# Performance work log

Hardware: AMD Instinct MI355X
Metric: run time of the kernel (lower is better)

The kernel has to match this reference:

```python
import jax, jax.numpy as jnp
import numpy as np

EMBED_DIM = 1024
NUM_HEADS = 16
HEAD_DIM = EMBED_DIM // NUM_HEADS

# Hamilton-product combination tensor C[out_comp, weight_comp, in_comp]
_C = np.zeros((4, 4, 4), dtype=np.float32)
for o, terms in enumerate([
    [(0, 0, 1), (1, 1, -1), (2, 2, -1), (3, 3, -1)],  # r_out
    [(1, 0, 1), (0, 1, 1), (3, 2, 1), (2, 3, -1)],    # i_out
    [(2, 0, 1), (3, 1, -1), (0, 2, 1), (1, 3, 1)],    # j_out
    [(3, 0, 1), (2, 1, 1), (1, 2, -1), (0, 3, 1)],    # k_out
]):
    for d, c, s in terms:
        _C[o, d, c] = s
C = jnp.asarray(_C)


def _xavier(key, shape):
    fan_in, fan_out = shape[-1], shape[-2]
    a = jnp.sqrt(6.0 / (fan_in + fan_out))
    return jax.random.uniform(key, shape, jnp.float32, -a, a)


def setup_inputs() -> dict:
    key = jax.random.key(0)
    ks = jax.random.split(key, 8)
    B, T, E = 4, 1024, EMBED_DIM
    inp = {
        'q': jax.random.normal(ks[0], (B, T, E, 4), jnp.float32),
        'k': jax.random.normal(ks[1], (B, T, E, 4), jnp.float32),
        'v': jax.random.normal(ks[2], (B, T, E, 4), jnp.float32),
    }
    for name, kk in zip(['Wq', 'Wk', 'Wv', 'Wo'], ks[3:7]):
        # stacked [r,i,j,k] weights, each (out_features, in_features)
        inp[name] = _xavier(kk, (4, E, E))
        inp[name.replace('W', 'b')] = jnp.zeros((E, 4), jnp.float32)
    return inp


def qlinear(x, W, b):
    # x: [B,T,in,4(c)], W: [4(d),out,in], b: [out,4]
    # effective block weight: Weff[q_out, c_in, out, in]
    Weff = jnp.einsum('doi,qdc->qcoi', W, C)
    out = jnp.einsum('btic,qcoi->btoq', x, Weff)
    return out + b  # bias broadcasts over B,T


def split_heads(x):
    B, T, D, Q = x.shape
    x = x.reshape(B, T, NUM_HEADS, HEAD_DIM, Q)
    return x.transpose(0, 2, 1, 3, 4)  # [B,H,T,hd,4]


def combine_heads(x):
    B, H, T, D, Q = x.shape
    return x.transpose(0, 2, 1, 3, 4).reshape(B, T, H * D, Q)


def reference(q, k, v, Wq, bq, Wk, bk, Wv, bv, Wo, bo):
    qh = split_heads(qlinear(q, Wq, bq))
    kh = split_heads(qlinear(k, Wk, bk))
    vh = split_heads(qlinear(v, Wv, bv))
    scale = 1.0 / jnp.sqrt(jnp.float32(HEAD_DIM * 4))
    scores = jnp.einsum('bhqfd,bhkfd->bhqk', qh, kh) * scale
    attn = jax.nn.softmax(scores, axis=-1)
    out = jnp.einsum('bhqk,bhkfd->bhqfd', attn, vh)
    return qlinear(combine_heads(out), Wo, bo)
```

## Files before the change

### kernel.cpp

```cpp
#include <hip/hip_runtime.h>
#include <hip/hip_bf16.h>

typedef _Float16 h16;
typedef h16   h16x8 __attribute__((ext_vector_type(8)));
typedef h16   h16x4 __attribute__((ext_vector_type(4)));
typedef float f32x4 __attribute__((ext_vector_type(4)));

#define EMB 1024
#define ED4 4096L

__device__ __forceinline__ void gload_lds16(const void* g, void* l) {
    __builtin_amdgcn_global_load_lds(
        (__attribute__((address_space(1))) void*)g,
        (__attribute__((address_space(3))) void*)l,
        16, 0, 0);
}

__global__ __launch_bounds__(256) void k_build_m(const float* __restrict__ W, h16* __restrict__ M) {
    int t = blockIdx.x * 256 + threadIdx.x;
    int i = t & 1023;
    int n = t >> 10;
    int o = n >> 2, q = n & 3;
    unsigned packed = 0xEu | (0x8u << 4) | (0x2u << 8) | (0x4u << 12);
    unsigned sm = (packed >> (q * 4)) & 0xFu;
    h16x4 out;
#pragma unroll
    for (int c = 0; c < 4; ++c) {
        int d = q ^ c;
        float w = W[((long)d * EMB + o) * EMB + i];
        out[c] = (h16)(((sm >> c) & 1u) ? -w : w);
    }
    *(h16x4*)&M[(long)n * ED4 + i * 4] = out;
}

__global__ __launch_bounds__(256) void k_f32_to_f16(const float* __restrict__ in, h16* __restrict__ out) {
    long i = ((long)blockIdx.x * 256 + threadIdx.x) * 4;
    float4 v = *(const float4*)(in + i);
    h16x4 o;
    o[0] = (h16)v.x; o[1] = (h16)v.y; o[2] = (h16)v.z; o[3] = (h16)v.w;
    *(h16x4*)(out + i) = o;
}

#define BAR() __builtin_amdgcn_s_barrier()
#define LGKM0() do { asm volatile("s_waitcnt lgkmcnt(0)" ::: "memory"); \
                     __builtin_amdgcn_sched_barrier(0); } while (0)
#define STAGE(matv, basev, row0v, tt, hh) do { \
    const h16* _src = (basev) + ((row0v) + (hh) * 128L) * 4096L + (long)(tt) * 64 + scol; \
    h16* _dst = &lds[(((tt) & 1) << 15) + (matv) * 16384 + (hh) * 8192 + w * 512]; \
    gload_lds16(_src, _dst); \
    gload_lds16(_src + 64 * 4096L, _dst + 4096); \
} while (0)
#define LDA_(mh, m, ks) (*(const h16x8*)&lds[cb + (mh) * 8192 + (wm * 64 + (m) * 16 + fr) * 64 + ((((ks) * 4 + kq) ^ fr7) << 3)])
#define LDB_(nh, n, ks) (*(const h16x8*)&lds[cb + 16384 + (nh) * 8192 + (wn * 32 + (n) * 16 + fr) * 64 + ((((ks) * 4 + kq) ^ fr7) << 3)])
#define MFMA_Q(MH, NH, BF) do { \
    __builtin_amdgcn_s_setprio(1); \
    _Pragma("unroll") \
    for (int m = 0; m < 4; ++m) \
        _Pragma("unroll") \
        for (int n = 0; n < 2; ++n) { \
            acc[MH][NH][m][n] = __builtin_amdgcn_mfma_f32_16x16x32_f16(af[m][0], BF[n][0], acc[MH][NH][m][n], 0, 0, 0); \
            acc[MH][NH][m][n] = __builtin_amdgcn_mfma_f32_16x16x32_f16(af[m][1], BF[n][1], acc[MH][NH][m][n], 0, 0, 0); \
        } \
    __builtin_amdgcn_s_setprio(0); \
} while (0)

template <typename OUT_T>
__global__ __launch_bounds__(512, 2) void k_gemm256(
    const h16* __restrict__ A, const h16* __restrict__ B,
    OUT_T* __restrict__ C, const float* __restrict__ bias, int nt)
{
    __shared__ __align__(16) h16 lds[65536];

    const int tid = threadIdx.x;
    const int w  = tid >> 6, l = tid & 63;
    const int wm = w >> 2, wn = w & 3;
    const int fr = l & 15, fr7 = l & 7, kq = l >> 4;

    const int srow = w * 8 + (l >> 3);
    const int scol = ((l & 7) ^ ((l >> 3) & 7)) << 3;
    const long arow0 = (long)blockIdx.x * 256 + srow;
    const long brow0 = (long)blockIdx.y * 256 + srow;

    f32x4 acc[2][2][4][2] = {};

    STAGE(0, A, arow0, 0, 0);
    STAGE(1, B, brow0, 0, 0);
    STAGE(0, A, arow0, 0, 1);
    STAGE(1, B, brow0, 0, 1);
    STAGE(0, A, arow0, 1, 0);
    STAGE(1, B, brow0, 1, 0);
    asm volatile("s_waitcnt vmcnt(4)" ::: "memory");
    __builtin_amdgcn_sched_barrier(0);
    BAR();

    for (int t = 0; t < nt; ++t) {
        const int cb = (t & 1) << 15;
        h16x8 af[4][2], b0[2][2], b1[2][2];

#pragma unroll
        for (int m = 0; m < 4; ++m) { af[m][0] = LDA_(0, m, 0); af[m][1] = LDA_(0, m, 1); }
#pragma unroll
        for (int n = 0; n < 2; ++n) { b0[n][0] = LDB_(0, n, 0); b0[n][1] = LDB_(0, n, 1); }
        if (t + 1 < nt) STAGE(0, A, arow0, t + 1, 1);
        BAR(); LGKM0();
        MFMA_Q(0, 0, b0);
        BAR();

#pragma unroll
        for (int n = 0; n < 2; ++n) { b1[n][0] = LDB_(1, n, 0); b1[n][1] = LDB_(1, n, 1); }
        if (t + 1 < nt) STAGE(1, B, brow0, t + 1, 1);
        BAR(); LGKM0();
        MFMA_Q(0, 1, b1);
        BAR();

#pragma unroll
        for (int m = 0; m < 4; ++m) { af[m][0] = LDA_(1, m, 0); af[m][1] = LDA_(1, m, 1); }
        if (t + 2 < nt) STAGE(0, A, arow0, t + 2, 0);
        BAR(); LGKM0();
        MFMA_Q(1, 0, b0);
        BAR();

        if (t + 2 < nt) STAGE(1, B, brow0, t + 2, 0);
        if (t < nt - 2) { asm volatile("s_waitcnt vmcnt(4)" ::: "memory"); }
        else            { asm volatile("s_waitcnt vmcnt(0)" ::: "memory"); }
        __builtin_amdgcn_sched_barrier(0);
        BAR();
        MFMA_Q(1, 1, b1);
        BAR();
    }

    const long row00 = (long)blockIdx.x * 256 + wm * 64 + kq * 4;
    const int  col00 = (int)blockIdx.y * 256 + wn * 32 + fr;
#pragma unroll
    for (int mh = 0; mh < 2; ++mh)
#pragma unroll
        for (int nh = 0; nh < 2; ++nh)
#pragma unroll
            for (int n = 0; n < 2; ++n) {
                const int col = col00 + nh * 128 + n * 16;
                const float bv = bias[col];
#pragma unroll
                for (int m = 0; m < 4; ++m) {
                    const long r0 = row00 + mh * 128 + m * 16;
#pragma unroll
                    for (int j = 0; j < 4; ++j)
                        C[(r0 + j) * 4096L + col] = (OUT_T)(acc[mh][nh][m][n][j] + bv);
                }
            }
}

template <typename OUT_T, bool HAS_BIAS>
__global__ __launch_bounds__(256) void k_gemm_bt(
    const h16* __restrict__ A, const h16* __restrict__ B,
    OUT_T* __restrict__ C, const float* __restrict__ bias,
    int lda, int ldb, int ldc,
    long sAb, long sAh, long sBb, long sBh, long sCb, long sCh,
    float alpha, int kIters)
{
    __shared__ __align__(16) h16 As[128 * 32];
    __shared__ __align__(16) h16 Bs[128 * 32];

    const int z = blockIdx.z, zb = z >> 4, zh = z & 15;
    const h16* Ab = A + zb * sAb + zh * sAh + (long)blockIdx.x * 128 * lda;
    const h16* Bb = B + zb * sBb + zh * sBh + (long)blockIdx.y * 128 * ldb;

    const int tid = threadIdx.x, w = tid >> 6, lane = tid & 63;
    const int wr = (w >> 1) * 64, wc = (w & 1) * 64;
    const int scol = (lane & 3) * 8;
    const int srow = lane >> 2;
    const int koff = (lane >> 4) * 8;
    const int fr   = lane & 15;

    f32x4 acc[4][4] = {};

    for (int kt = 0; kt < kIters; ++kt) {
        const int k0 = kt * 32;
#pragma unroll
        for (int j = 0; j < 2; ++j) {
            const int ca  = w * 2 + j;
            const int row = ca * 16 + srow;
            gload_lds16(Ab + (long)row * lda + k0 + scol, &As[ca * 512]);
            gload_lds16(Bb + (long)row * ldb + k0 + scol, &Bs[ca * 512]);
        }
        __syncthreads();

        h16x8 af[4], bfr[4];
#pragma unroll
        for (int m = 0; m < 4; ++m)
            af[m] = *(const h16x8*)&As[(wr + m * 16 + fr) * 32 + koff];
#pragma unroll
        for (int n = 0; n < 4; ++n)
            bfr[n] = *(const h16x8*)&Bs[(wc + n * 16 + fr) * 32 + koff];
        __syncthreads();

#pragma unroll
        for (int m = 0; m < 4; ++m)
#pragma unroll
            for (int n = 0; n < 4; ++n)
                acc[m][n] = __builtin_amdgcn_mfma_f32_16x16x32_f16(af[m], bfr[n], acc[m][n], 0, 0, 0);
    }

    OUT_T* Cb = C + zb * sCb + zh * sCh;
    const long rbase = (long)blockIdx.x * 128 + wr + (lane >> 4) * 4;
    const int  cbase = blockIdx.y * 128 + wc + fr;
#pragma unroll
    for (int n = 0; n < 4; ++n) {
        const int col = cbase + n * 16;
        const float bv = HAS_BIAS ? bias[col] : 0.0f;
#pragma unroll
        for (int m = 0; m < 4; ++m) {
            const long row0 = rbase + m * 16;
#pragma unroll
            for (int j = 0; j < 4; ++j) {
                float vv = acc[m][n][j] * alpha + bv;
                Cb[(row0 + j) * ldc + col] = (OUT_T)vv;
            }
        }
    }
}

__global__ void k_transpose_v(const h16* __restrict__ Vb, h16* __restrict__ Vt) {
    __shared__ h16 tile[32][34];
    const int z = blockIdx.z, b = z >> 4, h = z & 15;
    const int f0 = blockIdx.x * 32, t0 = blockIdx.y * 32;
    const int tx = threadIdx.x, ty = threadIdx.y;
#pragma unroll
    for (int j = 0; j < 4; ++j)
        tile[ty + 8 * j][tx] = Vb[(long)(b * 1024 + t0 + ty + 8 * j) * ED4 + h * 256 + f0 + tx];
    __syncthreads();
#pragma unroll
    for (int j = 0; j < 4; ++j)
        Vt[(long)z * (256 * 1024) + (long)(f0 + ty + 8 * j) * 1024 + t0 + tx] = tile[tx][ty + 8 * j];
}

__global__ __launch_bounds__(256) void k_softmax(h16* __restrict__ S) {
    const long row = blockIdx.x;
    h16* p = S + row * 1024;
    const int tid = threadIdx.x, w = tid >> 6, lane = tid & 63;
    h16x4 xi = *(const h16x4*)&p[tid * 4];
    float x[4];
#pragma unroll
    for (int j = 0; j < 4; ++j) x[j] = (float)xi[j];
    float m = fmaxf(fmaxf(x[0], x[1]), fmaxf(x[2], x[3]));
#pragma unroll
    for (int off = 32; off; off >>= 1) m = fmaxf(m, __shfl_xor(m, off));
    __shared__ float red[8];
    if (lane == 0) red[w] = m;
    __syncthreads();
    m = fmaxf(fmaxf(red[0], red[1]), fmaxf(red[2], red[3]));
    float s = 0.0f;
#pragma unroll
    for (int j = 0; j < 4; ++j) { x[j] = __expf(x[j] - m); s += x[j]; }
#pragma unroll
    for (int off = 32; off; off >>= 1) s += __shfl_xor(s, off);
    if (lane == 0) red[4 + w] = s;
    __syncthreads();
    s = red[4] + red[5] + red[6] + red[7];
    const float inv = 1.0f / s;
    h16x4 o;
#pragma unroll
    for (int j = 0; j < 4; ++j) o[j] = (h16)(x[j] * inv);
    *(h16x4*)&p[tid * 4] = o;
}

extern "C" void kernel_launch(void* const* d_in, const int* in_sizes, int n_in,
                              void* d_out, int out_size, void* d_ws, size_t ws_size,
                              hipStream_t stream) {
    const float* q  = (const float*)d_in[0];
    const float* k  = (const float*)d_in[1];
    const float* v  = (const float*)d_in[2];
    const float* Wq = (const float*)d_in[3];
    const float* bq = (const float*)d_in[4];
    const float* Wk = (const float*)d_in[5];
    const float* bk = (const float*)d_in[6];
    const float* Wv = (const float*)d_in[7];
    const float* bv = (const float*)d_in[8];
    const float* Wo = (const float*)d_in[9];
    const float* bo = (const float*)d_in[10];
    float* out = (float*)d_out;

    char* ws = (char*)d_ws;
    const long MB = 1024L * 1024;
    h16* X  = (h16*)(ws + 0 * MB);
    h16* M  = (h16*)(ws + 32 * MB);
    h16* Qb = (h16*)(ws + 64 * MB);
    h16* Kb = (h16*)(ws + 96 * MB);
    h16* Vb = (h16*)(ws + 128 * MB);
    h16* Vt = (h16*)(ws + 160 * MB);
    h16* AO = (h16*)(ws + 192 * MB);
    h16* Sc = (h16*)(ws + 224 * MB);

    dim3 blk(256);
    dim3 g256(16, 16, 1);

    k_f32_to_f16<<<16384, blk, 0, stream>>>(q, X);
    k_build_m<<<16384, blk, 0, stream>>>(Wq, M);
    k_gemm256<h16><<<g256, 512, 0, stream>>>(X, M, Qb, bq, 64);

    k_f32_to_f16<<<16384, blk, 0, stream>>>(k, X);
    k_build_m<<<16384, blk, 0, stream>>>(Wk, M);
    k_gemm256<h16><<<g256, 512, 0, stream>>>(X, M, Kb, bk, 64);

    k_f32_to_f16<<<16384, blk, 0, stream>>>(v, X);
    k_build_m<<<16384, blk, 0, stream>>>(Wv, M);
    k_gemm256<h16><<<g256, 512, 0, stream>>>(X, M, Vb, bv, 64);

    k_transpose_v<<<dim3(8, 32, 64), dim3(32, 8), 0, stream>>>(Vb, Vt);

    for (int c = 0; c < 4; ++c) {
        const h16* Qc  = Qb + (long)c * 1024 * 4096;
        const h16* Kc  = Kb + (long)c * 1024 * 4096;
        const h16* VtC = Vt + (long)c * 16 * 256 * 1024;
        h16*       AOc = AO + (long)c * 1024 * 4096;

        k_gemm_bt<h16, false><<<dim3(8, 8, 16), blk, 0, stream>>>(
            Qc, Kc, Sc, nullptr,
            4096, 4096, 1024,
            0, 256,
            0, 256,
            0, 1024L * 1024,
            0.0625f, 8);

        k_softmax<<<16384, blk, 0, stream>>>(Sc);

        k_gemm_bt<h16, false><<<dim3(8, 2, 16), blk, 0, stream>>>(
            Sc, VtC, AOc, nullptr,
            1024, 1024, 4096,
            0, 1024L * 1024,
            0, 256L * 1024,
            0, 256,
            1.0f, 32);
    }

    k_build_m<<<16384, blk, 0, stream>>>(Wo, M);
    k_gemm256<float><<<g256, 512, 0, stream>>>(AO, M, out, bo, 64);
}
```

Baseline: 908.7 us.

## Switch projection GEMM to 32x32x16 MFMA and add swizzled block-to-tile mapping

```diff
diff --git a/kernel.cpp b/kernel.cpp
--- a/kernel.cpp
+++ b/kernel.cpp
@@ -5,6 +5,7 @@
 typedef h16   h16x8 __attribute__((ext_vector_type(8)));
 typedef h16   h16x4 __attribute__((ext_vector_type(4)));
 typedef float f32x4 __attribute__((ext_vector_type(4)));
+typedef float f32x16 __attribute__((ext_vector_type(16)));
 
 #define EMB 1024
 #define ED4 4096L
@@ -50,17 +51,15 @@
     gload_lds16(_src, _dst); \
     gload_lds16(_src + 64 * 4096L, _dst + 4096); \
 } while (0)
-#define LDA_(mh, m, ks) (*(const h16x8*)&lds[cb + (mh) * 8192 + (wm * 64 + (m) * 16 + fr) * 64 + ((((ks) * 4 + kq) ^ fr7) << 3)])
-#define LDB_(nh, n, ks) (*(const h16x8*)&lds[cb + 16384 + (nh) * 8192 + (wn * 32 + (n) * 16 + fr) * 64 + ((((ks) * 4 + kq) ^ fr7) << 3)])
-#define MFMA_Q(MH, NH, BF) do { \
+#define LDA32(mh, mf, ks) (*(const h16x8*)&lds[cbuf + (mh) * 8192 + (wm * 64 + (mf) * 32 + l31) * 64 + ((((ks) * 2 + lhi) ^ l7) << 3)])
+#define LDB32(nh, ks)     (*(const h16x8*)&lds[cbuf + 16384 + (nh) * 8192 + (wn * 32 + l31) * 64 + ((((ks) * 2 + lhi) ^ l7) << 3)])
+#define MFMA_Q32(MH, NH, BF) do { \
     __builtin_amdgcn_s_setprio(1); \
     _Pragma("unroll") \
-    for (int m = 0; m < 4; ++m) \
+    for (int ks = 0; ks < 4; ++ks) \
         _Pragma("unroll") \
-        for (int n = 0; n < 2; ++n) { \
-            acc[MH][NH][m][n] = __builtin_amdgcn_mfma_f32_16x16x32_f16(af[m][0], BF[n][0], acc[MH][NH][m][n], 0, 0, 0); \
-            acc[MH][NH][m][n] = __builtin_amdgcn_mfma_f32_16x16x32_f16(af[m][1], BF[n][1], acc[MH][NH][m][n], 0, 0, 0); \
-        } \
+        for (int mf = 0; mf < 2; ++mf) \
+            acc[MH][NH][mf] = __builtin_amdgcn_mfma_f32_32x32x16_f16(af[mf][ks], BF[ks], acc[MH][NH][mf], 0, 0, 0); \
     __builtin_amdgcn_s_setprio(0); \
 } while (0)
 
@@ -74,14 +73,18 @@
     const int tid = threadIdx.x;
     const int w  = tid >> 6, l = tid & 63;
     const int wm = w >> 2, wn = w & 3;
-    const int fr = l & 15, fr7 = l & 7, kq = l >> 4;
+    const int l31 = l & 31, lhi = l >> 5, l7 = l & 7;
+
+    const int wid0 = blockIdx.y * 16 + blockIdx.x;
+    const int wid  = (wid0 & 7) * 32 + (wid0 >> 3);
+    const int tx = wid & 15, ty = wid >> 4;
 
     const int srow = w * 8 + (l >> 3);
     const int scol = ((l & 7) ^ ((l >> 3) & 7)) << 3;
-    const long arow0 = (long)blockIdx.x * 256 + srow;
-    const long brow0 = (long)blockIdx.y * 256 + srow;
-
-    f32x4 acc[2][2][4][2] = {};
+    const long arow0 = (long)tx * 256 + srow;
+    const long brow0 = (long)ty * 256 + srow;
+
+    f32x16 acc[2][2][2] = {};
 
     STAGE(0, A, arow0, 0, 0);
     STAGE(1, B, brow0, 0, 0);
@@ -94,30 +97,34 @@
     BAR();
 
     for (int t = 0; t < nt; ++t) {
-        const int cb = (t & 1) << 15;
-        h16x8 af[4][2], b0[2][2], b1[2][2];
-
-#pragma unroll
-        for (int m = 0; m < 4; ++m) { af[m][0] = LDA_(0, m, 0); af[m][1] = LDA_(0, m, 1); }
-#pragma unroll
-        for (int n = 0; n < 2; ++n) { b0[n][0] = LDB_(0, n, 0); b0[n][1] = LDB_(0, n, 1); }
+        const int cbuf = (t & 1) << 15;
+        h16x8 af[2][4], b0[4], b1[4];
+
+#pragma unroll
+        for (int mf = 0; mf < 2; ++mf)
+#pragma unroll
+            for (int ks = 0; ks < 4; ++ks) af[mf][ks] = LDA32(0, mf, ks);
+#pragma unroll
+        for (int ks = 0; ks < 4; ++ks) b0[ks] = LDB32(0, ks);
         if (t + 1 < nt) STAGE(0, A, arow0, t + 1, 1);
         BAR(); LGKM0();
-        MFMA_Q(0, 0, b0);
-        BAR();
-
-#pragma unroll
-        for (int n = 0; n < 2; ++n) { b1[n][0] = LDB_(1, n, 0); b1[n][1] = LDB_(1, n, 1); }
+        MFMA_Q32(0, 0, b0);
+        BAR();
+
+#pragma unroll
+        for (int ks = 0; ks < 4; ++ks) b1[ks] = LDB32(1, ks);
         if (t + 1 < nt) STAGE(1, B, brow0, t + 1, 1);
         BAR(); LGKM0();
-        MFMA_Q(0, 1, b1);
-        BAR();
-
-#pragma unroll
-        for (int m = 0; m < 4; ++m) { af[m][0] = LDA_(1, m, 0); af[m][1] = LDA_(1, m, 1); }
+        MFMA_Q32(0, 1, b1);
+        BAR();
+
+#pragma unroll
+        for (int mf = 0; mf < 2; ++mf)
+#pragma unroll
+            for (int ks = 0; ks < 4; ++ks) af[mf][ks] = LDA32(1, mf, ks);
         if (t + 2 < nt) STAGE(0, A, arow0, t + 2, 0);
         BAR(); LGKM0();
-        MFMA_Q(1, 0, b0);
+        MFMA_Q32(1, 0, b0);
         BAR();
 
         if (t + 2 < nt) STAGE(1, B, brow0, t + 2, 0);
@@ -125,28 +132,28 @@
         else            { asm volatile("s_waitcnt vmcnt(0)" ::: "memory"); }
         __builtin_amdgcn_sched_barrier(0);
         BAR();
-        MFMA_Q(1, 1, b1);
-        BAR();
-    }
-
-    const long row00 = (long)blockIdx.x * 256 + wm * 64 + kq * 4;
-    const int  col00 = (int)blockIdx.y * 256 + wn * 32 + fr;
+        MFMA_Q32(1, 1, b1);
+        BAR();
+    }
+
+    const long rb  = (long)tx * 256 + wm * 64 + 4 * lhi;
+    const int  cb0 = ty * 256 + wn * 32 + l31;
 #pragma unroll
     for (int mh = 0; mh < 2; ++mh)
 #pragma unroll
-        for (int nh = 0; nh < 2; ++nh)
-#pragma unroll
-            for (int n = 0; n < 2; ++n) {
-                const int col = col00 + nh * 128 + n * 16;
-                const float bv = bias[col];
-#pragma unroll
-                for (int m = 0; m < 4; ++m) {
-                    const long r0 = row00 + mh * 128 + m * 16;
-#pragma unroll
-                    for (int j = 0; j < 4; ++j)
-                        C[(r0 + j) * 4096L + col] = (OUT_T)(acc[mh][nh][m][n][j] + bv);
+        for (int nh = 0; nh < 2; ++nh) {
+            const int col = cb0 + nh * 128;
+            const float bv = bias[col];
+#pragma unroll
+            for (int mf = 0; mf < 2; ++mf) {
+                const long r0 = rb + mh * 128 + mf * 32;
+#pragma unroll
+                for (int j = 0; j < 16; ++j) {
+                    const long row = r0 + (j & 3) + 8 * (j >> 2);
+                    C[row * 4096L + col] = (OUT_T)(acc[mh][nh][mf][j] + bv);
                 }
             }
+        }
 }
 
 template <typename OUT_T, bool HAS_BIAS>
```

New measurement: 979.5 us. +7.8%, slower.
